# Kernel optimization log

Measured on AMD Instinct MI355X. Metric: run time of the kernel, lower is better.

The kernel has to match this reference:

```python
import jax, jax.numpy as jnp
import numpy as np

N, E = 50000, 800000
H, C = 4, 32          # heads, channels -> concat dim 128
ED = 8                # edge_dim
NREL = 16             # n_relations
LAYERS = 3
MLP_HID = 100
NEG_SLOPE = 0.2


def setup_inputs():
    key = jax.random.key(0)
    ks = jax.random.split(key, 16)
    s = 0.1
    return {
        "x": jax.random.normal(ks[0], (N, 1), jnp.float32),
        "edge_index": jax.random.randint(ks[1], (2, E), 0, N),
        "edge_type": jax.random.randint(ks[2], (E,), 0, NREL),
        "edge_emb": jax.random.normal(ks[3], (NREL, ED), jnp.float32) * s,
        "W_l0": jax.random.normal(ks[4], (C, H * C), jnp.float32) * s,
        "W_l1": jax.random.normal(ks[5], (H * C, H * C), jnp.float32) * s,
        "W_l2": jax.random.normal(ks[6], (H * C, H * C), jnp.float32) * s,
        "att_src": jax.random.normal(ks[7], (LAYERS, H, C), jnp.float32) * s,
        "att_dst": jax.random.normal(ks[8], (LAYERS, H, C), jnp.float32) * s,
        "att_edge": jax.random.normal(ks[9], (LAYERS, H, C), jnp.float32) * s,
        "W_edge": jax.random.normal(ks[10], (LAYERS, ED, H * C), jnp.float32) * s,
        "bias": jax.random.normal(ks[11], (LAYERS, H * C), jnp.float32) * s,
        "mlp_W1": jax.random.normal(ks[12], (H * C, MLP_HID), jnp.float32) * s,
        "mlp_b1": jnp.zeros((MLP_HID,), jnp.float32),
        "mlp_W2": jax.random.normal(ks[13], (MLP_HID, 1), jnp.float32) * s,
        "mlp_b2": jnp.zeros((1,), jnp.float32),
    }


def _gat_layer(x, src, dst, edge_attr, W, a_src, a_dst, a_edge, We, b):
    # PyG GATConv: shared lin for src/dst, additive attention + edge attr term
    n = x.shape[0]
    h = (x @ W).reshape(n, H, C)                      # [N,H,C]
    e = (edge_attr @ We).reshape(-1, H, C)            # [E',H,C]
    s_src = (h * a_src).sum(-1)                       # [N,H]
    s_dst = (h * a_dst).sum(-1)                       # [N,H]
    s_edge = (e * a_edge).sum(-1)                     # [E',H]
    alpha = jax.nn.leaky_relu(s_src[src] + s_dst[dst] + s_edge, NEG_SLOPE)
    # softmax over incoming edges of each destination node
    amax = jax.ops.segment_max(alpha, dst, num_segments=n)
    ealpha = jnp.exp(alpha - amax[dst])
    denom = jax.ops.segment_sum(ealpha, dst, num_segments=n)
    alpha = ealpha / (denom[dst] + 1e-16)             # [E',H]
    msg = h[src] * alpha[:, :, None]                  # [E',H,C]
    out = jax.ops.segment_sum(msg, dst, num_segments=n)
    return out.reshape(n, H * C) + b


def _forward(x, edge_index, edge_type, edge_emb, W_l0, W_l1, W_l2,
             att_src, att_dst, att_edge, W_edge, bias,
             mlp_W1, mlp_b1, mlp_W2, mlp_b2):
    n = x.shape[0]
    x = jnp.broadcast_to(x, (n, C))                   # x.expand(-1, channels)
    src, dst = edge_index[0], edge_index[1]
    loop = jnp.arange(n)
    src_f = jnp.concatenate([src, loop])              # add_self_loops
    dst_f = jnp.concatenate([dst, loop])
    Ws = [W_l0, W_l1, W_l2]
    for i in range(LAYERS):
        edge_attr = edge_emb[edge_type]               # [E,ED]
        fill = jnp.broadcast_to(edge_attr.mean(0), (n, ED))  # fill_value='mean'
        edge_attr_f = jnp.concatenate([edge_attr, fill], axis=0)
        xl = x
        x = _gat_layer(x, src_f, dst_f, edge_attr_f, Ws[i],
                       att_src[i], att_dst[i], att_edge[i], W_edge[i], bias[i])
        if i > 0:
            x = x + xl                                # residual (i>0 only)
        x = jax.nn.relu(x)                            # nonlin; norm='none'
    h = jax.nn.relu(x @ mlp_W1 + mlp_b1)
    return jax.nn.sigmoid(h @ mlp_W2 + mlp_b2)        # [N,1]


def reference(x, edge_index, edge_type, edge_emb, W_l0, W_l1, W_l2,
              att_src, att_dst, att_edge, W_edge, bias,
              mlp_W1, mlp_b1, mlp_W2, mlp_b2):
    return _forward(x, edge_index, edge_type, edge_emb, W_l0, W_l1, W_l2,
                    att_src, att_dst, att_edge, W_edge, bias,
                    mlp_W1, mlp_b1, mlp_W2, mlp_b2)
```

## Files before the change

kernel.cpp:

```cpp
#include <hip/hip_runtime.h>
#include <hip/hip_bf16.h>
#include <hip/hip_fp16.h>

#define HCONC 128
#define NHEAD 4
#define CCH   32
#define EDIM  8
#define NREL  16
#define BCAP  5120
#define TILE  2048

typedef float floatx2 __attribute__((ext_vector_type(2)));
typedef short bf16x8 __attribute__((ext_vector_type(8)));
typedef float f32x4 __attribute__((ext_vector_type(4)));

__device__ inline unsigned short pack_fp8x2(float a, float b) {
    return (unsigned short)(__builtin_amdgcn_cvt_pk_fp8_f32(a, b, 0, false) & 0xFFFF);
}
__device__ inline unsigned pack_bf2(float lo, float hi) {
    __hip_bfloat162 v;
    v.x = __float2bfloat16(lo);
    v.y = __float2bfloat16(hi);
    return *(unsigned*)&v;
}

__global__ __launch_bounds__(256) void binA_kernel(
    const int* __restrict__ ei, const int* __restrict__ etype, int E, int nbuk, int nA,
    int* __restrict__ gcursor, int* __restrict__ cnt, unsigned* __restrict__ ebuf,
    const float* __restrict__ W_l1, const float* __restrict__ W_l2,
    const float* __restrict__ mW1,
    unsigned* __restrict__ Wl1q, unsigned* __restrict__ Wl2q, unsigned* __restrict__ W1q,
    const float* __restrict__ W_l0, const float* __restrict__ emb,
    const float* __restrict__ att_src, const float* __restrict__ att_dst,
    const float* __restrict__ att_edge, const float* __restrict__ W_edge,
    float* __restrict__ W0s, float* __restrict__ SA0, float* __restrict__ SD0,
    float* __restrict__ stab) {
    __shared__ int hist[256], lbase[256], gbase[256], tmp[256];
    __shared__ int lcnt16[NREL];
    __shared__ unsigned srt[TILE];
    __shared__ unsigned char sbuk[TILE];
    __shared__ float W0s_s[HCONC];
    int t = threadIdx.x;

    if ((int)blockIdx.x >= nA) {
        int pb = (int)blockIdx.x - nA;
        if (pb == 92) {
            if (t < HCONC) {
                float s = 0.f;
                for (int k = 0; k < CCH; k++) s += W_l0[k * HCONC + t];
                W0s[t] = s; W0s_s[t] = s;
            }
            __syncthreads();
            if (t < NHEAD) {
                float sa = 0.f, sd = 0.f;
                for (int c = 0; c < CCH; c++) {
                    sa += W0s_s[t * CCH + c] * att_src[t * CCH + c];
                    sd += W0s_s[t * CCH + c] * att_dst[t * CCH + c];
                }
                SA0[t] = sa; SD0[t] = sd;
            }
            if (t < 192) {
                int l = t >> 6, rem = t & 63, typ = rem >> 2, hh = rem & 3;
                const float* attr = emb + typ * EDIM;
                const float* We = W_edge + l * EDIM * HCONC;
                const float* ae = att_edge + l * HCONC + hh * CCH;
                float s = 0.f;
                for (int c = 0; c < CCH; c++) {
                    float ev = 0.f;
                    for (int dd = 0; dd < EDIM; dd++)
                        ev += attr[dd] * We[dd * HCONC + hh * CCH + c];
                    s += ev * ae[c];
                }
                stab[l * 68 + typ * 4 + hh] = s;
            }
            return;
        }
        int i = pb * 256 + t;
        if (i < 16384) {
            const float* W = (i < 8192) ? W_l1 : W_l2;
            unsigned* dst = (i < 8192) ? Wl1q : Wl2q;
            int r = i & 8191;
            int j2 = r & 3, lane = (r >> 2) & 63, kb = (r >> 8) & 3, tt = r >> 10;
            int k0 = kb * 32 + ((lane >> 4) & 3) * 8 + 2 * j2;
            int c = 16 * tt + (lane & 15);
            dst[r] = pack_bf2(W[k0 * 128 + c], W[(k0 + 1) * 128 + c]);
        } else if (i < 16384 + 7168) {
            int r = i - 16384;
            int j2 = r & 3, lane = (r >> 2) & 63, kb = (r >> 8) & 3, tt = r >> 10;
            int k0 = kb * 32 + ((lane >> 4) & 3) * 8 + 2 * j2;
            int c = 16 * tt + (lane & 15);
            float lo = (c < 100) ? mW1[k0 * 100 + c] : 0.f;
            float hi = (c < 100) ? mW1[(k0 + 1) * 100 + c] : 0.f;
            W1q[r] = pack_bf2(lo, hi);
        }
        return;
    }

    hist[t] = 0;
    if (t < NREL) lcnt16[t] = 0;
    __syncthreads();

    int base = blockIdx.x * TILE;
    int count = min(TILE, E - base);

    unsigned rec[8]; int slot[8]; int buk[8];
#pragma unroll
    for (int i = 0; i < 8; i++) {
        int idx = t + i * 256;
        if (idx < count) {
            int g = base + idx;
            int s = ei[g], d = ei[E + g], ty = etype[g];
            rec[i] = (unsigned)s | ((unsigned)ty << 16) | ((unsigned)(d & 255) << 20);
            buk[i] = d >> 8;
            slot[i] = atomicAdd(&hist[buk[i]], 1);
            atomicAdd(&lcnt16[ty], 1);
        } else buk[i] = -1;
    }
    __syncthreads();

    int v = hist[t];
    tmp[t] = v; __syncthreads();
    for (int off = 1; off < 256; off <<= 1) {
        int add = (t >= off) ? tmp[t - off] : 0; __syncthreads();
        tmp[t] += add; __syncthreads();
    }
    lbase[t] = tmp[t] - v;
    if (t < nbuk && v > 0) gbase[t] = atomicAdd(&gcursor[t], v);
    __syncthreads();

#pragma unroll
    for (int i = 0; i < 8; i++)
        if (buk[i] >= 0) {
            int pos = lbase[buk[i]] + slot[i];
            srt[pos] = rec[i];
            sbuk[pos] = (unsigned char)buk[i];
        }
    if (t < NREL) atomicAdd(&cnt[t], lcnt16[t]);
    __syncthreads();

    for (int idx = t; idx < count; idx += 256) {
        unsigned r = srt[idx];
        int bk = sbuk[idx];
        int rel = gbase[bk] + idx - lbase[bk];
        if (rel < BCAP) ebuf[bk * BCAP + rel] = r;
    }
}

__global__ __launch_bounds__(256) void binB_kernel(
    const unsigned* __restrict__ ebuf, const int* __restrict__ gcursor,
    int n, int nbuk,
    int* __restrict__ row_ptr, unsigned* __restrict__ col,
    const int* __restrict__ cnt, float* __restrict__ stab, int E,
    const float* __restrict__ x,
    const float* __restrict__ SA0, const float* __restrict__ SD0,
    float* __restrict__ val0) {
    __shared__ int hist[256], lcur[256], tmp[256];
    __shared__ unsigned colsl[BCAP];
    __shared__ __align__(16) float stab0[68];
    int b = blockIdx.x, t = threadIdx.x;

    if (t < 64) stab0[t] = stab[t];
    float invE = 1.f / (float)E;
    if (t < 4) {
        float s = 0.f;
        for (int r = 0; r < NREL; r++) s += (float)cnt[r] * stab[r * 4 + t];
        stab0[64 + t] = s * invE;
    }

    int c = (t < nbuk) ? gcursor[t] : 0;
    tmp[t] = c; __syncthreads();
    for (int off = 1; off < 256; off <<= 1) {
        int add = (t >= off) ? tmp[t - off] : 0; __syncthreads();
        tmp[t] += add; __syncthreads();
    }
    int gstart = (b == 0) ? 0 : tmp[b - 1];
    if (b == 0 && t == nbuk - 1) row_ptr[n] = tmp[t];
    if (b == 0 && t < 12) {
        int l = t >> 2, hh = t & 3;
        float s = 0.f;
        for (int r = 0; r < NREL; r++) s += (float)cnt[r] * stab[l * 68 + r * 4 + hh];
        stab[l * 68 + 64 + hh] = s * invE;
    }
    __syncthreads();

    int bbase = b * BCAP;
    int cntb = min(gcursor[b], BCAP);
    hist[t] = 0;
    __syncthreads();
    for (int i = t; i < cntb; i += 256) {
        unsigned r = ebuf[bbase + i];
        atomicAdd(&hist[r >> 20], 1);
    }
    __syncthreads();
    int v = hist[t];
    tmp[t] = v; __syncthreads();
    for (int off = 1; off < 256; off <<= 1) {
        int add = (t >= off) ? tmp[t - off] : 0; __syncthreads();
        tmp[t] += add; __syncthreads();
    }
    lcur[t] = tmp[t] - v;
    int gdst = (b << 8) + t;
    if (gdst < n) row_ptr[gdst] = gstart + tmp[t] - v;
    __syncthreads();
    for (int i = t; i < cntb; i += 256) {
        unsigned r = ebuf[bbase + i];
        int pos = atomicAdd(&lcur[r >> 20], 1);
        colsl[pos] = r & 0xFFFFFu;
    }
    __syncthreads();
    for (int i = t; i < cntb; i += 256)
        col[gstart + i] = colsl[i];

    int lo = tmp[t] - v, hi = tmp[t];
    if (gdst < n) {
        float xd = x[gdst];
        float4 sa4 = *(const float4*)SA0;
        float4 sdc = *(const float4*)SD0;
        float sd0 = xd * sdc.x, sd1 = xd * sdc.y, sd2 = xd * sdc.z, sd3 = xd * sdc.w;
        float s0 = fmaf(xd, sa4.x, sd0) + stab0[64];
        float s1 = fmaf(xd, sa4.y, sd1) + stab0[65];
        float s2 = fmaf(xd, sa4.z, sd2) + stab0[66];
        float s3 = fmaf(xd, sa4.w, sd3) + stab0[67];
        s0 = s0 > 0.f ? s0 : 0.2f * s0;
        s1 = s1 > 0.f ? s1 : 0.2f * s1;
        s2 = s2 > 0.f ? s2 : 0.2f * s2;
        s3 = s3 > 0.f ? s3 : 0.2f * s3;
        float w0 = __expf(s0), w1 = __expf(s1), w2 = __expf(s2), w3 = __expf(s3);
        float den0 = w0, den1 = w1, den2 = w2, den3 = w3;
        float sx0 = w0 * xd, sx1 = w1 * xd, sx2 = w2 * xd, sx3 = w3 * xd;
        for (int j = lo; j < hi; j++) {
            unsigned p = colsl[j];
            float xv = x[p & 0xFFFFu];
            int typ = (int)(p >> 16);
            float4 st = *(const float4*)&stab0[typ * 4];
            float e0 = fmaf(xv, sa4.x, sd0) + st.x;
            float e1 = fmaf(xv, sa4.y, sd1) + st.y;
            float e2 = fmaf(xv, sa4.z, sd2) + st.z;
            float e3 = fmaf(xv, sa4.w, sd3) + st.w;
            e0 = e0 > 0.f ? e0 : 0.2f * e0;
            e1 = e1 > 0.f ? e1 : 0.2f * e1;
            e2 = e2 > 0.f ? e2 : 0.2f * e2;
            e3 = e3 > 0.f ? e3 : 0.2f * e3;
            float g0 = __expf(e0), g1 = __expf(e1), g2 = __expf(e2), g3 = __expf(e3);
            den0 += g0; den1 += g1; den2 += g2; den3 += g3;
            sx0 = fmaf(g0, xv, sx0); sx1 = fmaf(g1, xv, sx1);
            sx2 = fmaf(g2, xv, sx2); sx3 = fmaf(g3, xv, sx3);
        }
        float4 vo;
        vo.x = sx0 / (den0 + 1e-16f);
        vo.y = sx1 / (den1 + 1e-16f);
        vo.z = sx2 / (den2 + 1e-16f);
        vo.w = sx3 / (den3 + 1e-16f);
        ((float4*)val0)[gdst] = vo;
    }
}

__global__ __launch_bounds__(256, 2) void transform0_kernel(
    const float* __restrict__ val0, const float* __restrict__ W0s,
    const float* __restrict__ bias0, const unsigned* __restrict__ Wq,
    const float* __restrict__ a_src, const float* __restrict__ a_dst,
    unsigned short* __restrict__ h8, float* __restrict__ s_src,
    float* __restrict__ s_dst, int n) {
    __shared__ unsigned short hs[64 * 128];
    int tid = threadIdx.x;
    int lane = tid & 63;
    int wv = tid >> 6;
    int q = lane >> 4, nl = lane & 15;
    int row_blk = blockIdx.x * 64;
    int wrow = wv * 16;

    int arow = row_blk + wrow + nl;
    if (arow >= n) arow = n - 1;
    float4 v4 = ((const float4*)val0)[arow];

    f32x4 acc[8];
#pragma unroll
    for (int t = 0; t < 8; t++) acc[t] = (f32x4){0.f, 0.f, 0.f, 0.f};

    const uint4* Wp4 = (const uint4*)Wq;
#pragma unroll
    for (int kb = 0; kb < 4; kb++) {
        int c4 = 8 * kb + 2 * q;
        float4 wa = ((const float4*)W0s)[c4];
        float4 wb = ((const float4*)W0s)[c4 + 1];
        float4 ba = ((const float4*)bias0)[c4];
        float4 bb = ((const float4*)bias0)[c4 + 1];
        float vr = kb == 0 ? v4.x : kb == 1 ? v4.y : kb == 2 ? v4.z : v4.w;
        float x0 = fmaxf(fmaf(vr, wa.x, ba.x), 0.f);
        float x1 = fmaxf(fmaf(vr, wa.y, ba.y), 0.f);
        float x2 = fmaxf(fmaf(vr, wa.z, ba.z), 0.f);
        float x3 = fmaxf(fmaf(vr, wa.w, ba.w), 0.f);
        float x4 = fmaxf(fmaf(vr, wb.x, bb.x), 0.f);
        float x5 = fmaxf(fmaf(vr, wb.y, bb.y), 0.f);
        float x6 = fmaxf(fmaf(vr, wb.z, bb.z), 0.f);
        float x7 = fmaxf(fmaf(vr, wb.w, bb.w), 0.f);
        uint4 ua;
        ua.x = pack_bf2(x0, x1);
        ua.y = pack_bf2(x2, x3);
        ua.z = pack_bf2(x4, x5);
        ua.w = pack_bf2(x6, x7);
        bf16x8 af = __builtin_bit_cast(bf16x8, ua);
#pragma unroll
        for (int t = 0; t < 8; t++) {
            uint4 ub = Wp4[(t * 4 + kb) * 64 + lane];
            bf16x8 bf = __builtin_bit_cast(bf16x8, ub);
            acc[t] = __builtin_amdgcn_mfma_f32_16x16x32_bf16(af, bf, acc[t], 0, 0, 0);
        }
    }

    float av[8], dv[8];
#pragma unroll
    for (int t = 0; t < 8; t++) {
        av[t] = a_src[16 * t + nl];
        dv[t] = a_dst[16 * t + nl];
    }
#pragma unroll
    for (int reg = 0; reg < 4; reg++) {
        float t0 = acc[0][reg] * av[0] + acc[1][reg] * av[1];
        float t1 = acc[2][reg] * av[2] + acc[3][reg] * av[3];
        float t2 = acc[4][reg] * av[4] + acc[5][reg] * av[5];
        float t3 = acc[6][reg] * av[6] + acc[7][reg] * av[7];
        float d0 = acc[0][reg] * dv[0] + acc[1][reg] * dv[1];
        float d1 = acc[2][reg] * dv[2] + acc[3][reg] * dv[3];
        float d2 = acc[4][reg] * dv[4] + acc[5][reg] * dv[5];
        float d3 = acc[6][reg] * dv[6] + acc[7][reg] * dv[7];
#pragma unroll
        for (int off = 1; off <= 8; off <<= 1) {
            t0 += __shfl_xor(t0, off); t1 += __shfl_xor(t1, off);
            t2 += __shfl_xor(t2, off); t3 += __shfl_xor(t3, off);
            d0 += __shfl_xor(d0, off); d1 += __shfl_xor(d1, off);
            d2 += __shfl_xor(d2, off); d3 += __shfl_xor(d3, off);
        }
        int row = row_blk + wrow + q * 4 + reg;
        if (row < n && nl < 4) {
            float ts = nl == 0 ? t0 : nl == 1 ? t1 : nl == 2 ? t2 : t3;
            float td = nl == 0 ? d0 : nl == 1 ? d1 : nl == 2 ? d2 : d3;
            s_src[row * 4 + nl] = ts;
            s_dst[row * 4 + nl] = td;
        }
    }

#pragma unroll
    for (int t = 0; t < 8; t++) {
#pragma unroll
        for (int reg = 0; reg < 4; reg++) {
            __hip_bfloat16 b = __float2bfloat16(acc[t][reg]);
            hs[(wrow + q * 4 + reg) * 128 + 16 * t + nl] = *(unsigned short*)&b;
        }
    }
    __syncthreads();
    const unsigned* hsu = (const unsigned*)hs;
#pragma unroll
    for (int i = 0; i < 16; i++) {
        int pidx = tid + i * 256;
        int rl = pidx >> 6, cp = pidx & 63;
        int row = row_blk + rl;
        if (row < n) {
            unsigned u = hsu[rl * 64 + cp];
            float f0 = __uint_as_float(u << 16);
            float f1 = __uint_as_float(u & 0xFFFF0000u);
            h8[(size_t)row * 64 + cp] = pack_fp8x2(f0, f1);
        }
    }
}

__global__ __launch_bounds__(256) void agg_t_kernel(
    const unsigned char* __restrict__ h8, const float* __restrict__ s_src,
    const float* __restrict__ s_dst, const int* __restrict__ row_ptr,
    const unsigned* __restrict__ col, const float* __restrict__ tab,
    const float* __restrict__ bias, const float* __restrict__ val0,
    const float* __restrict__ W0s, const float* __restrict__ bias0,
    unsigned short* __restrict__ xb_out,
    const unsigned* __restrict__ Wq,
    const float* __restrict__ a_src2, const float* __restrict__ a_dst2,
    unsigned short* __restrict__ h8o, float* __restrict__ s_srco,
    float* __restrict__ s_dsto, int n) {
    __shared__ __align__(16) float stab_s[68];
    __shared__ __align__(16) unsigned short xrow[16 * 144];
    __shared__ __align__(4) unsigned short hs[16 * 130];
    if (threadIdx.x < 68) stab_s[threadIdx.x] = tab[threadIdx.x];
    __syncthreads();

    int tid = threadIdx.x;
    int lane = tid & 63;
    int wv = tid >> 6;
    int grp = lane >> 4;
    int l16 = lane & 15;
    int head = l16 >> 2;
    int dl = wv * 4 + grp;
    int d = blockIdx.x * 16 + dl;
    bool alive = d < n;
    int dc = alive ? d : n - 1;

    int start = row_ptr[dc];
    int end = alive ? row_ptr[dc + 1] : start;
    float sdh = s_dst[dc * 4 + head];

    float s = s_src[dc * 4 + head] + sdh + stab_s[64 + head];
    s = s > 0.f ? s : 0.2f * s;
    float w = __expf(s);
    uint2 u = ((const uint2*)(h8 + (size_t)dc * 128))[l16];
    floatx2 f01 = __builtin_amdgcn_cvt_pk_f32_fp8((int)u.x, false);
    floatx2 f23 = __builtin_amdgcn_cvt_pk_f32_fp8((int)u.x, true);
    floatx2 f45 = __builtin_amdgcn_cvt_pk_f32_fp8((int)u.y, false);
    floatx2 f67 = __builtin_amdgcn_cvt_pk_f32_fp8((int)u.y, true);
    float den = w;
    float a0 = w * f01.x, a1 = w * f01.y;
    float a2 = w * f23.x, a3 = w * f23.y;
    float a4 = w * f45.x, a5 = w * f45.y;
    float a6 = w * f67.x, a7 = w * f67.y;
#pragma unroll 4
    for (int e = start; e < end; e++) {
        unsigned pp = col[e];
        int esrc = (int)(pp & 0xFFFFu);
        int typ = (int)(pp >> 16);
        float sc = s_src[esrc * 4 + head] + sdh + stab_s[typ * 4 + head];
        sc = sc > 0.f ? sc : 0.2f * sc;
        float we = __expf(sc);
        uint2 ue = ((const uint2*)(h8 + (size_t)esrc * 128))[l16];
        floatx2 g01 = __builtin_amdgcn_cvt_pk_f32_fp8((int)ue.x, false);
        floatx2 g23 = __builtin_amdgcn_cvt_pk_f32_fp8((int)ue.x, true);
        floatx2 g45 = __builtin_amdgcn_cvt_pk_f32_fp8((int)ue.y, false);
        floatx2 g67 = __builtin_amdgcn_cvt_pk_f32_fp8((int)ue.y, true);
        den += we;
        a0 = fmaf(we, g01.x, a0);  a1 = fmaf(we, g01.y, a1);
        a2 = fmaf(we, g23.x, a2);  a3 = fmaf(we, g23.y, a3);
        a4 = fmaf(we, g45.x, a4);  a5 = fmaf(we, g45.y, a5);
        a6 = fmaf(we, g67.x, a6);  a7 = fmaf(we, g67.y, a7);
    }

    float inv = 1.f / (den + 1e-16f);
    float4 b0 = ((const float4*)bias)[2 * l16];
    float4 b1v = ((const float4*)bias)[2 * l16 + 1];
    float4 o0v, o1v;
    o0v.x = a0 * inv + b0.x;  o0v.y = a1 * inv + b0.y;
    o0v.z = a2 * inv + b0.z;  o0v.w = a3 * inv + b0.w;
    o1v.x = a4 * inv + b1v.x; o1v.y = a5 * inv + b1v.y;
    o1v.z = a6 * inv + b1v.z; o1v.w = a7 * inv + b1v.w;
    {
        float vv = val0[dc * 4 + head];
        float4 wa = ((const float4*)W0s)[2 * l16];
        float4 wb = ((const float4*)W0s)[2 * l16 + 1];
        float4 ba = ((const float4*)bias0)[2 * l16];
        float4 bb = ((const float4*)bias0)[2 * l16 + 1];
        o0v.x += fmaxf(fmaf(vv, wa.x, ba.x), 0.f);
        o0v.y += fmaxf(fmaf(vv, wa.y, ba.y), 0.f);
        o0v.z += fmaxf(fmaf(vv, wa.z, ba.z), 0.f);
        o0v.w += fmaxf(fmaf(vv, wa.w, ba.w), 0.f);
        o1v.x += fmaxf(fmaf(vv, wb.x, bb.x), 0.f);
        o1v.y += fmaxf(fmaf(vv, wb.y, bb.y), 0.f);
        o1v.z += fmaxf(fmaf(vv, wb.z, bb.z), 0.f);
        o1v.w += fmaxf(fmaf(vv, wb.w, bb.w), 0.f);
    }
    o0v.x = fmaxf(o0v.x, 0.f); o0v.y = fmaxf(o0v.y, 0.f);
    o0v.z = fmaxf(o0v.z, 0.f); o0v.w = fmaxf(o0v.w, 0.f);
    o1v.x = fmaxf(o1v.x, 0.f); o1v.y = fmaxf(o1v.y, 0.f);
    o1v.z = fmaxf(o1v.z, 0.f); o1v.w = fmaxf(o1v.w, 0.f);
    uint4 pk;
    pk.x = pack_bf2(o0v.x, o0v.y);
    pk.y = pack_bf2(o0v.z, o0v.w);
    pk.z = pack_bf2(o1v.x, o1v.y);
    pk.w = pack_bf2(o1v.z, o1v.w);
    if (alive) ((uint4*)xb_out)[(size_t)d * 16 + l16] = pk;
    *(uint4*)&xrow[dl * 144 + l16 * 8] = pk;
    __syncthreads();

    int lo = 2 * wv, hi = lo + 1;
    f32x4 aL = (f32x4){0.f, 0.f, 0.f, 0.f};
    f32x4 aH = (f32x4){0.f, 0.f, 0.f, 0.f};
    const uint4* Wp4 = (const uint4*)Wq;
#pragma unroll
    for (int kb = 0; kb < 4; kb++) {
        bf16x8 af = __builtin_bit_cast(bf16x8,
            *(const uint4*)&xrow[l16 * 144 + kb * 32 + grp * 8]);
        bf16x8 bL = __builtin_bit_cast(bf16x8, Wp4[(lo * 4 + kb) * 64 + lane]);
        bf16x8 bH = __builtin_bit_cast(bf16x8, Wp4[(hi * 4 + kb) * 64 + lane]);
        aL = __builtin_amdgcn_mfma_f32_16x16x32_bf16(af, bL, aL, 0, 0, 0);
        aH = __builtin_amdgcn_mfma_f32_16x16x32_bf16(af, bH, aH, 0, 0, 0);
    }
    float avl = a_src2[32 * wv + l16], avh = a_src2[32 * wv + 16 + l16];
    float dvl = a_dst2[32 * wv + l16], dvh = a_dst2[32 * wv + 16 + l16];
#pragma unroll
    for (int reg = 0; reg < 4; reg++) {
        float ps = aL[reg] * avl + aH[reg] * avh;
        float pd = aL[reg] * dvl + aH[reg] * dvh;
#pragma unroll
        for (int off = 1; off <= 8; off <<= 1) {
            ps += __shfl_xor(ps, off);
            pd += __shfl_xor(pd, off);
        }
        int rg = blockIdx.x * 16 + grp * 4 + reg;
        if (l16 == 0 && rg < n) {
            s_srco[rg * 4 + wv] = ps;
            s_dsto[rg * 4 + wv] = pd;
        }
        __hip_bfloat16 bLh = __float2bfloat16(aL[reg]);
        __hip_bfloat16 bHh = __float2bfloat16(aH[reg]);
        hs[(grp * 4 + reg) * 130 + 16 * lo + l16] = *(unsigned short*)&bLh;
        hs[(grp * 4 + reg) * 130 + 16 * hi + l16] = *(unsigned short*)&bHh;
    }
    __syncthreads();
#pragma unroll
    for (int i = 0; i < 4; i++) {
        int pidx = tid + i * 256;
        int rl = pidx >> 6, cp = pidx & 63;
        int rg = blockIdx.x * 16 + rl;
        if (rg < n) {
            unsigned uu = *(const unsigned*)&hs[rl * 130 + cp * 2];
            float f0 = __uint_as_float(uu << 16);
            float f1 = __uint_as_float(uu & 0xFFFF0000u);
            h8o[(size_t)rg * 64 + cp] = pack_fp8x2(f0, f1);
        }
    }
}

__global__ __launch_bounds__(256) void agg_m_kernel(
    const unsigned char* __restrict__ h8, const float* __restrict__ s_src,
    const float* __restrict__ s_dst, const int* __restrict__ row_ptr,
    const unsigned* __restrict__ col, const float* __restrict__ tab,
    const float* __restrict__ bias, const unsigned short* __restrict__ x_prev,
    const unsigned* __restrict__ W1q, const float* __restrict__ b1,
    const float* __restrict__ W2, const float* __restrict__ b2,
    float* __restrict__ out, int n) {
    __shared__ __align__(16) float stab_s[68];
    __shared__ __align__(16) unsigned short xrow[16 * 144];
    __shared__ float partial[16][4];
    if (threadIdx.x < 68) stab_s[threadIdx.x] = tab[threadIdx.x];
    __syncthreads();

    int tid = threadIdx.x;
    int lane = tid & 63;
    int wv = tid >> 6;
    int grp = lane >> 4;
    int l16 = lane & 15;
    int head = l16 >> 2;
    int dl = wv * 4 + grp;
    int d = blockIdx.x * 16 + dl;
    bool alive = d < n;
    int dc = alive ? d : n - 1;

    int start = row_ptr[dc];
    int end = alive ? row_ptr[dc + 1] : start;
    float sdh = s_dst[dc * 4 + head];

    float s = s_src[dc * 4 + head] + sdh + stab_s[64 + head];
    s = s > 0.f ? s : 0.2f * s;
    float w = __expf(s);
    uint2 u = ((const uint2*)(h8 + (size_t)dc * 128))[l16];
    floatx2 f01 = __builtin_amdgcn_cvt_pk_f32_fp8((int)u.x, false);
    floatx2 f23 = __builtin_amdgcn_cvt_pk_f32_fp8((int)u.x, true);
    floatx2 f45 = __builtin_amdgcn_cvt_pk_f32_fp8((int)u.y, false);
    floatx2 f67 = __builtin_amdgcn_cvt_pk_f32_fp8((int)u.y, true);
    float den = w;
    float a0 = w * f01.x, a1 = w * f01.y;
    float a2 = w * f23.x, a3 = w * f23.y;
    float a4 = w * f45.x, a5 = w * f45.y;
    float a6 = w * f67.x, a7 = w * f67.y;
#pragma unroll 4
    for (int e = start; e < end; e++) {
        unsigned pp = col[e];
        int esrc = (int)(pp & 0xFFFFu);
        int typ = (int)(pp >> 16);
        float sc = s_src[esrc * 4 + head] + sdh + stab_s[typ * 4 + head];
        sc = sc > 0.f ? sc : 0.2f * sc;
        float we = __expf(sc);
        uint2 ue = ((const uint2*)(h8 + (size_t)esrc * 128))[l16];
        floatx2 g01 = __builtin_amdgcn_cvt_pk_f32_fp8((int)ue.x, false);
        floatx2 g23 = __builtin_amdgcn_cvt_pk_f32_fp8((int)ue.x, true);
        floatx2 g45 = __builtin_amdgcn_cvt_pk_f32_fp8((int)ue.y, false);
        floatx2 g67 = __builtin_amdgcn_cvt_pk_f32_fp8((int)ue.y, true);
        den += we;
        a0 = fmaf(we, g01.x, a0);  a1 = fmaf(we, g01.y, a1);
        a2 = fmaf(we, g23.x, a2);  a3 = fmaf(we, g23.y, a3);
        a4 = fmaf(we, g45.x, a4);  a5 = fmaf(we, g45.y, a5);
        a6 = fmaf(we, g67.x, a6);  a7 = fmaf(we, g67.y, a7);
    }

    float inv = 1.f / (den + 1e-16f);
    float4 b0 = ((const float4*)bias)[2 * l16];
    float4 b1v = ((const float4*)bias)[2 * l16 + 1];
    float4 o0v, o1v;
    o0v.x = a0 * inv + b0.x;  o0v.y = a1 * inv + b0.y;
    o0v.z = a2 * inv + b0.z;  o0v.w = a3 * inv + b0.w;
    o1v.x = a4 * inv + b1v.x; o1v.y = a5 * inv + b1v.y;
    o1v.z = a6 * inv + b1v.z; o1v.w = a7 * inv + b1v.w;
    {
        uint4 pr = ((const uint4*)x_prev)[(size_t)dc * 16 + l16];
        o0v.x += __uint_as_float(pr.x << 16);
        o0v.y += __uint_as_float(pr.x & 0xFFFF0000u);
        o0v.z += __uint_as_float(pr.y << 16);
        o0v.w += __uint_as_float(pr.y & 0xFFFF0000u);
        o1v.x += __uint_as_float(pr.z << 16);
        o1v.y += __uint_as_float(pr.z & 0xFFFF0000u);
        o1v.z += __uint_as_float(pr.w << 16);
        o1v.w += __uint_as_float(pr.w & 0xFFFF0000u);
    }
    o0v.x = fmaxf(o0v.x, 0.f); o0v.y = fmaxf(o0v.y, 0.f);
    o0v.z = fmaxf(o0v.z, 0.f); o0v.w = fmaxf(o0v.w, 0.f);
    o1v.x = fmaxf(o1v.x, 0.f); o1v.y = fmaxf(o1v.y, 0.f);
    o1v.z = fmaxf(o1v.z, 0.f); o1v.w = fmaxf(o1v.w, 0.f);
    uint4 pk;
    pk.x = pack_bf2(o0v.x, o0v.y);
    pk.y = pack_bf2(o0v.z, o0v.w);
    pk.z = pack_bf2(o1v.x, o1v.y);
    pk.w = pack_bf2(o1v.z, o1v.w);
    *(uint4*)&xrow[dl * 144 + l16 * 8] = pk;
    __syncthreads();

    int lo = 2 * wv;
    bool two = wv < 3;
    f32x4 aL = (f32x4){0.f, 0.f, 0.f, 0.f};
    f32x4 aH = (f32x4){0.f, 0.f, 0.f, 0.f};
    const uint4* Wp4 = (const uint4*)W1q;
#pragma unroll
    for (int kb = 0; kb < 4; kb++) {
        bf16x8 af = __builtin_bit_cast(bf16x8,
            *(const uint4*)&xrow[l16 * 144 + kb * 32 + grp * 8]);
        bf16x8 bL = __builtin_bit_cast(bf16x8, Wp4[(lo * 4 + kb) * 64 + lane]);
        aL = __builtin_amdgcn_mfma_f32_16x16x32_bf16(af, bL, aL, 0, 0, 0);
        if (two) {
            bf16x8 bH = __builtin_bit_cast(bf16x8, Wp4[((lo + 1) * 4 + kb) * 64 + lane]);
            aH = __builtin_amdgcn_mfma_f32_16x16x32_bf16(af, bH, aH, 0, 0, 0);
        }
    }
    int cL = 16 * lo + l16;
    float b1L = (cL < 100) ? b1[cL] : 0.f;
    float w2L = (cL < 100) ? W2[cL] : 0.f;
    float b1H = 0.f, w2H = 0.f;
    if (two) {
        int cH = cL + 16;
        b1H = (cH < 100) ? b1[cH] : 0.f;
        w2H = (cH < 100) ? W2[cH] : 0.f;
    }
#pragma unroll
    for (int reg = 0; reg < 4; reg++) {
        float psum = fmaxf(aL[reg] + b1L, 0.f) * w2L;
        if (two) psum = fmaf(fmaxf(aH[reg] + b1H, 0.f), w2H, psum);
#pragma unroll
        for (int off = 1; off <= 8; off <<= 1)
            psum += __shfl_xor(psum, off);
        if (l16 == 0) partial[grp * 4 + reg][wv] = psum;
    }
    __syncthreads();
    if (tid < 16) {
        int rg = blockIdx.x * 16 + tid;
        if (rg < n) {
            float sum = partial[tid][0] + partial[tid][1] +
                        partial[tid][2] + partial[tid][3] + b2[0];
            out[rg] = 1.f / (1.f + __expf(-sum));
        }
    }
}

extern "C" void kernel_launch(void* const* d_in, const int* in_sizes, int n_in,
                              void* d_out, int out_size, void* d_ws, size_t ws_size,
                              hipStream_t stream) {
    const float* x       = (const float*)d_in[0];
    const int*   ei      = (const int*)d_in[1];
    const int*   etype   = (const int*)d_in[2];
    const float* emb     = (const float*)d_in[3];
    const float* W_l0    = (const float*)d_in[4];
    const float* W_l1    = (const float*)d_in[5];
    const float* W_l2    = (const float*)d_in[6];
    const float* att_src = (const float*)d_in[7];
    const float* att_dst = (const float*)d_in[8];
    const float* att_edge= (const float*)d_in[9];
    const float* W_edge  = (const float*)d_in[10];
    const float* bias    = (const float*)d_in[11];
    const float* mW1     = (const float*)d_in[12];
    const float* mb1     = (const float*)d_in[13];
    const float* mW2     = (const float*)d_in[14];
    const float* mb2     = (const float*)d_in[15];

    int n = in_sizes[0];
    int E = in_sizes[2];
    int nbuk = (n + 255) >> 8;
    int nA = (E + TILE - 1) / TILE;

    float* p   = (float*)d_ws;
    float* xb  = p; p += (size_t)n * 64;
    float* ssrc = p; p += (size_t)n * NHEAD;
    float* sdst = p; p += (size_t)n * NHEAD;
    float* ssrc2 = p; p += (size_t)n * NHEAD;
    float* sdst2 = p; p += (size_t)n * NHEAD;
    float* val0 = p; p += (size_t)n * NHEAD;
    float* hbf  = p; p += (size_t)n * 32;
    float* hbf2 = p; p += (size_t)n * 32;
    unsigned* Wl1q = (unsigned*)p; p += 8192;
    unsigned* Wl2q = (unsigned*)p; p += 8192;
    unsigned* W1q  = (unsigned*)p; p += 7168;
    int* row_ptr     = (int*)p;
    int* gcursor     = row_ptr + n + 1;
    int* cnt         = gcursor + 256;
    float* W0s    = (float*)(cnt + 16);
    float* SA0    = W0s + HCONC;
    float* SD0    = SA0 + NHEAD;
    float* meanat = SD0 + NHEAD;
    float* stab   = meanat + EDIM;
    char* raw = (char*)(stab + 256);
    unsigned* ebuf = (unsigned*)(((uintptr_t)raw + 15) & ~(uintptr_t)15);
    unsigned* col = ebuf + (size_t)nbuk * BCAP;

    (void)hipMemsetAsync(gcursor, 0, (256 + 16) * sizeof(int), stream);
    binA_kernel<<<nA + 93, 256, 0, stream>>>(ei, etype, E, nbuk, nA, gcursor, cnt,
                                             ebuf, W_l1, W_l2, mW1, Wl1q, Wl2q, W1q,
                                             W_l0, emb, att_src, att_dst, att_edge,
                                             W_edge, W0s, SA0, SD0, stab);
    binB_kernel<<<nbuk, 256, 0, stream>>>(ebuf, gcursor, n, nbuk, row_ptr, col,
                                          cnt, stab, E, x, SA0, SD0, val0);

    transform0_kernel<<<(n + 63) / 64, 256, 0, stream>>>(val0, W0s, bias + 0, Wl1q,
                                                         att_src + 128, att_dst + 128,
                                                         (unsigned short*)hbf, ssrc, sdst, n);
    agg_t_kernel<<<(n + 15) / 16, 256, 0, stream>>>(
        (const unsigned char*)hbf, ssrc, sdst, row_ptr, col,
        stab + 68, bias + 128, val0, W0s, bias + 0,
        (unsigned short*)xb, Wl2q, att_src + 256, att_dst + 256,
        (unsigned short*)hbf2, ssrc2, sdst2, n);
    agg_m_kernel<<<(n + 15) / 16, 256, 0, stream>>>(
        (const unsigned char*)hbf2, ssrc2, sdst2, row_ptr, col,
        stab + 136, bias + 256, (const unsigned short*)xb,
        W1q, mb1, mW2, mb2, (float*)d_out, n);
}
```

Before: 202.7 us.

## Fuse layer-0 transform into binning kernel and stage edge columns in LDS

The separate transform0 kernel is merged into binB. Each binB block keeps its 256 layer-0 aggregated values in shared memory and runs the MFMA transform over four 64-row phases, which removes one launch and the val0 reload. The agg_t and agg_m kernels also preload their block's contiguous column-index range into shared memory (up to 1024 entries) before the edge loop. In exchange, binB uses more LDS and runs with only 196 blocks, which limits parallelism for the transform work. The aggregation kernels also gain an extra barrier and a per-edge branch.

```diff
diff --git a/kernel.cpp b/kernel.cpp
--- a/kernel.cpp
+++ b/kernel.cpp
@@ -9,6 +9,7 @@
 #define NREL  16
 #define BCAP  5120
 #define TILE  2048
+#define CCAP  1024
 
 typedef float floatx2 __attribute__((ext_vector_type(2)));
 typedef short bf16x8 __attribute__((ext_vector_type(8)));
@@ -153,10 +154,18 @@
     const int* __restrict__ cnt, float* __restrict__ stab, int E,
     const float* __restrict__ x,
     const float* __restrict__ SA0, const float* __restrict__ SD0,
-    float* __restrict__ val0) {
+    float* __restrict__ val0,
+    const float* __restrict__ W0s, const float* __restrict__ bias0,
+    const unsigned* __restrict__ Wq,
+    const float* __restrict__ a_src, const float* __restrict__ a_dst,
+    unsigned short* __restrict__ h8, float* __restrict__ s_src,
+    float* __restrict__ s_dst) {
     __shared__ int hist[256], lcur[256], tmp[256];
     __shared__ unsigned colsl[BCAP];
     __shared__ __align__(16) float stab0[68];
+    __shared__ __align__(16) float vls[256][4];
+    __shared__ __align__(16) float W0s_s[HCONC], b0_s[HCONC];
+    __shared__ unsigned short hs[64 * 128];
     int b = blockIdx.x, t = threadIdx.x;
 
     if (t < 64) stab0[t] = stab[t];
@@ -166,6 +175,7 @@
         for (int r = 0; r < NREL; r++) s += (float)cnt[r] * stab[r * 4 + t];
         stab0[64 + t] = s * invE;
     }
+    if (t < HCONC) { W0s_s[t] = W0s[t]; b0_s[t] = bias0[t]; }
 
     int c = (t < nbuk) ? gcursor[t] : 0;
     tmp[t] = c; __syncthreads();
@@ -211,7 +221,8 @@
     for (int i = t; i < cntb; i += 256)
         col[gstart + i] = colsl[i];
 
-    int lo = tmp[t] - v, hi = tmp[t];
+    int lo0 = tmp[t] - v, hi0 = tmp[t];
+    float4 vo = make_float4(0.f, 0.f, 0.f, 0.f);
     if (gdst < n) {
         float xd = x[gdst];
         float4 sa4 = *(const float4*)SA0;
@@ -228,7 +239,7 @@
         float w0 = __expf(s0), w1 = __expf(s1), w2 = __expf(s2), w3 = __expf(s3);
         float den0 = w0, den1 = w1, den2 = w2, den3 = w3;
         float sx0 = w0 * xd, sx1 = w1 * xd, sx2 = w2 * xd, sx3 = w3 * xd;
-        for (int j = lo; j < hi; j++) {
+        for (int j = lo0; j < hi0; j++) {
             unsigned p = colsl[j];
             float xv = x[p & 0xFFFFu];
             int typ = (int)(p >> 16);
@@ -246,121 +257,111 @@
             sx0 = fmaf(g0, xv, sx0); sx1 = fmaf(g1, xv, sx1);
             sx2 = fmaf(g2, xv, sx2); sx3 = fmaf(g3, xv, sx3);
         }
-        float4 vo;
         vo.x = sx0 / (den0 + 1e-16f);
         vo.y = sx1 / (den1 + 1e-16f);
         vo.z = sx2 / (den2 + 1e-16f);
         vo.w = sx3 / (den3 + 1e-16f);
         ((float4*)val0)[gdst] = vo;
     }
-}
-
-__global__ __launch_bounds__(256, 2) void transform0_kernel(
-    const float* __restrict__ val0, const float* __restrict__ W0s,
-    const float* __restrict__ bias0, const unsigned* __restrict__ Wq,
-    const float* __restrict__ a_src, const float* __restrict__ a_dst,
-    unsigned short* __restrict__ h8, float* __restrict__ s_src,
-    float* __restrict__ s_dst, int n) {
-    __shared__ unsigned short hs[64 * 128];
-    int tid = threadIdx.x;
-    int lane = tid & 63;
-    int wv = tid >> 6;
+    *(float4*)vls[t] = vo;
+    __syncthreads();
+
+    int lane = t & 63, wvv = t >> 6;
     int q = lane >> 4, nl = lane & 15;
-    int row_blk = blockIdx.x * 64;
-    int wrow = wv * 16;
-
-    int arow = row_blk + wrow + nl;
-    if (arow >= n) arow = n - 1;
-    float4 v4 = ((const float4*)val0)[arow];
-
-    f32x4 acc[8];
-#pragma unroll
-    for (int t = 0; t < 8; t++) acc[t] = (f32x4){0.f, 0.f, 0.f, 0.f};
-
     const uint4* Wp4 = (const uint4*)Wq;
-#pragma unroll
-    for (int kb = 0; kb < 4; kb++) {
-        int c4 = 8 * kb + 2 * q;
-        float4 wa = ((const float4*)W0s)[c4];
-        float4 wb = ((const float4*)W0s)[c4 + 1];
-        float4 ba = ((const float4*)bias0)[c4];
-        float4 bb = ((const float4*)bias0)[c4 + 1];
-        float vr = kb == 0 ? v4.x : kb == 1 ? v4.y : kb == 2 ? v4.z : v4.w;
-        float x0 = fmaxf(fmaf(vr, wa.x, ba.x), 0.f);
-        float x1 = fmaxf(fmaf(vr, wa.y, ba.y), 0.f);
-        float x2 = fmaxf(fmaf(vr, wa.z, ba.z), 0.f);
-        float x3 = fmaxf(fmaf(vr, wa.w, ba.w), 0.f);
-        float x4 = fmaxf(fmaf(vr, wb.x, bb.x), 0.f);
-        float x5 = fmaxf(fmaf(vr, wb.y, bb.y), 0.f);
-        float x6 = fmaxf(fmaf(vr, wb.z, bb.z), 0.f);
-        float x7 = fmaxf(fmaf(vr, wb.w, bb.w), 0.f);
-        uint4 ua;
-        ua.x = pack_bf2(x0, x1);
-        ua.y = pack_bf2(x2, x3);
-        ua.z = pack_bf2(x4, x5);
-        ua.w = pack_bf2(x6, x7);
-        bf16x8 af = __builtin_bit_cast(bf16x8, ua);
-#pragma unroll
-        for (int t = 0; t < 8; t++) {
-            uint4 ub = Wp4[(t * 4 + kb) * 64 + lane];
-            bf16x8 bf = __builtin_bit_cast(bf16x8, ub);
-            acc[t] = __builtin_amdgcn_mfma_f32_16x16x32_bf16(af, bf, acc[t], 0, 0, 0);
-        }
-    }
-
     float av[8], dv[8];
 #pragma unroll
-    for (int t = 0; t < 8; t++) {
-        av[t] = a_src[16 * t + nl];
-        dv[t] = a_dst[16 * t + nl];
-    }
-#pragma unroll
-    for (int reg = 0; reg < 4; reg++) {
-        float t0 = acc[0][reg] * av[0] + acc[1][reg] * av[1];
-        float t1 = acc[2][reg] * av[2] + acc[3][reg] * av[3];
-        float t2 = acc[4][reg] * av[4] + acc[5][reg] * av[5];
-        float t3 = acc[6][reg] * av[6] + acc[7][reg] * av[7];
-        float d0 = acc[0][reg] * dv[0] + acc[1][reg] * dv[1];
-        float d1 = acc[2][reg] * dv[2] + acc[3][reg] * dv[3];
-        float d2 = acc[4][reg] * dv[4] + acc[5][reg] * dv[5];
-        float d3 = acc[6][reg] * dv[6] + acc[7][reg] * dv[7];
-#pragma unroll
-        for (int off = 1; off <= 8; off <<= 1) {
-            t0 += __shfl_xor(t0, off); t1 += __shfl_xor(t1, off);
-            t2 += __shfl_xor(t2, off); t3 += __shfl_xor(t3, off);
-            d0 += __shfl_xor(d0, off); d1 += __shfl_xor(d1, off);
-            d2 += __shfl_xor(d2, off); d3 += __shfl_xor(d3, off);
-        }
-        int row = row_blk + wrow + q * 4 + reg;
-        if (row < n && nl < 4) {
-            float ts = nl == 0 ? t0 : nl == 1 ? t1 : nl == 2 ? t2 : t3;
-            float td = nl == 0 ? d0 : nl == 1 ? d1 : nl == 2 ? d2 : d3;
-            s_src[row * 4 + nl] = ts;
-            s_dst[row * 4 + nl] = td;
-        }
-    }
-
-#pragma unroll
-    for (int t = 0; t < 8; t++) {
+    for (int tt = 0; tt < 8; tt++) {
+        av[tt] = a_src[16 * tt + nl];
+        dv[tt] = a_dst[16 * tt + nl];
+    }
+    for (int ph = 0; ph < 4; ph++) {
+        int wrow = wvv * 16;
+        int lrow = ph * 64 + wrow + nl;
+        float4 v4 = *(const float4*)vls[lrow];
+
+        f32x4 acc[8];
+#pragma unroll
+        for (int tt = 0; tt < 8; tt++) acc[tt] = (f32x4){0.f, 0.f, 0.f, 0.f};
+#pragma unroll
+        for (int kb = 0; kb < 4; kb++) {
+            int c4 = 8 * kb + 2 * q;
+            float4 wa = ((const float4*)W0s_s)[c4];
+            float4 wb = ((const float4*)W0s_s)[c4 + 1];
+            float4 ba = ((const float4*)b0_s)[c4];
+            float4 bb = ((const float4*)b0_s)[c4 + 1];
+            float vr = kb == 0 ? v4.x : kb == 1 ? v4.y : kb == 2 ? v4.z : v4.w;
+            float x0 = fmaxf(fmaf(vr, wa.x, ba.x), 0.f);
+            float x1 = fmaxf(fmaf(vr, wa.y, ba.y), 0.f);
+            float x2 = fmaxf(fmaf(vr, wa.z, ba.z), 0.f);
+            float x3 = fmaxf(fmaf(vr, wa.w, ba.w), 0.f);
+            float x4 = fmaxf(fmaf(vr, wb.x, bb.x), 0.f);
+            float x5 = fmaxf(fmaf(vr, wb.y, bb.y), 0.f);
+            float x6 = fmaxf(fmaf(vr, wb.z, bb.z), 0.f);
+            float x7 = fmaxf(fmaf(vr, wb.w, bb.w), 0.f);
+            uint4 ua;
+            ua.x = pack_bf2(x0, x1);
+            ua.y = pack_bf2(x2, x3);
+            ua.z = pack_bf2(x4, x5);
+            ua.w = pack_bf2(x6, x7);
+            bf16x8 af = __builtin_bit_cast(bf16x8, ua);
+#pragma unroll
+            for (int tt = 0; tt < 8; tt++) {
+                uint4 ub = Wp4[(tt * 4 + kb) * 64 + lane];
+                bf16x8 bf = __builtin_bit_cast(bf16x8, ub);
+                acc[tt] = __builtin_amdgcn_mfma_f32_16x16x32_bf16(af, bf, acc[tt], 0, 0, 0);
+            }
+        }
+
 #pragma unroll
         for (int reg = 0; reg < 4; reg++) {
-            __hip_bfloat16 b = __float2bfloat16(acc[t][reg]);
-            hs[(wrow + q * 4 + reg) * 128 + 16 * t + nl] = *(unsigned short*)&b;
-        }
-    }
-    __syncthreads();
-    const unsigned* hsu = (const unsigned*)hs;
-#pragma unroll
-    for (int i = 0; i < 16; i++) {
-        int pidx = tid + i * 256;
-        int rl = pidx >> 6, cp = pidx & 63;
-        int row = row_blk + rl;
-        if (row < n) {
-            unsigned u = hsu[rl * 64 + cp];
-            float f0 = __uint_as_float(u << 16);
-            float f1 = __uint_as_float(u & 0xFFFF0000u);
-            h8[(size_t)row * 64 + cp] = pack_fp8x2(f0, f1);
-        }
+            float t0 = acc[0][reg] * av[0] + acc[1][reg] * av[1];
+            float t1 = acc[2][reg] * av[2] + acc[3][reg] * av[3];
+            float t2 = acc[4][reg] * av[4] + acc[5][reg] * av[5];
+            float t3 = acc[6][reg] * av[6] + acc[7][reg] * av[7];
+            float d0 = acc[0][reg] * dv[0] + acc[1][reg] * dv[1];
+            float d1 = acc[2][reg] * dv[2] + acc[3][reg] * dv[3];
+            float d2 = acc[4][reg] * dv[4] + acc[5][reg] * dv[5];
+            float d3 = acc[6][reg] * dv[6] + acc[7][reg] * dv[7];
+#pragma unroll
+            for (int off = 1; off <= 8; off <<= 1) {
+                t0 += __shfl_xor(t0, off); t1 += __shfl_xor(t1, off);
+                t2 += __shfl_xor(t2, off); t3 += __shfl_xor(t3, off);
+                d0 += __shfl_xor(d0, off); d1 += __shfl_xor(d1, off);
+                d2 += __shfl_xor(d2, off); d3 += __shfl_xor(d3, off);
+            }
+            int grow = (b << 8) + ph * 64 + wrow + q * 4 + reg;
+            if (grow < n && nl < 4) {
+                float ts = nl == 0 ? t0 : nl == 1 ? t1 : nl == 2 ? t2 : t3;
+                float td = nl == 0 ? d0 : nl == 1 ? d1 : nl == 2 ? d2 : d3;
+                s_src[grow * 4 + nl] = ts;
+                s_dst[grow * 4 + nl] = td;
+            }
+        }
+
+#pragma unroll
+        for (int tt = 0; tt < 8; tt++) {
+#pragma unroll
+            for (int reg = 0; reg < 4; reg++) {
+                __hip_bfloat16 bh = __float2bfloat16(acc[tt][reg]);
+                hs[(wrow + q * 4 + reg) * 128 + 16 * tt + nl] = *(unsigned short*)&bh;
+            }
+        }
+        __syncthreads();
+        const unsigned* hsu = (const unsigned*)hs;
+#pragma unroll
+        for (int i = 0; i < 16; i++) {
+            int pidx = t + i * 256;
+            int rl = pidx >> 6, cp = pidx & 63;
+            int grow = (b << 8) + ph * 64 + rl;
+            if (grow < n) {
+                unsigned u = hsu[rl * 64 + cp];
+                float f0 = __uint_as_float(u << 16);
+                float f1 = __uint_as_float(u & 0xFFFF0000u);
+                h8[(size_t)grow * 64 + cp] = pack_fp8x2(f0, f1);
+            }
+        }
+        __syncthreads();
     }
 }
 
@@ -378,10 +379,21 @@
     __shared__ __align__(16) float stab_s[68];
     __shared__ __align__(16) unsigned short xrow[16 * 144];
     __shared__ __align__(4) unsigned short hs[16 * 130];
-    if (threadIdx.x < 68) stab_s[threadIdx.x] = tab[threadIdx.x];
-    __syncthreads();
-
+    __shared__ unsigned cols_s[CCAP];
+    __shared__ int ebb[2];
     int tid = threadIdx.x;
+    if (tid < 68) stab_s[tid] = tab[tid];
+    if (tid < 2) {
+        int ridx = (int)blockIdx.x * 16 + tid * 16;
+        if (ridx > n) ridx = n;
+        ebb[tid] = row_ptr[ridx];
+    }
+    __syncthreads();
+    int ebase = ebb[0];
+    int etot = ebb[1] - ebase;
+    for (int i = tid; i < etot && i < CCAP; i += 256) cols_s[i] = col[ebase + i];
+    __syncthreads();
+
     int lane = tid & 63;
     int wv = tid >> 6;
     int grp = lane >> 4;
@@ -411,7 +423,8 @@
     float a6 = w * f67.x, a7 = w * f67.y;
 #pragma unroll 4
     for (int e = start; e < end; e++) {
-        unsigned pp = col[e];
+        int ei_ = e - ebase;
+        unsigned pp = (ei_ < CCAP) ? cols_s[ei_] : col[e];
         int esrc = (int)(pp & 0xFFFFu);
         int typ = (int)(pp >> 16);
         float sc = s_src[esrc * 4 + head] + sdh + stab_s[typ * 4 + head];
@@ -525,10 +538,21 @@
     __shared__ __align__(16) float stab_s[68];
     __shared__ __align__(16) unsigned short xrow[16 * 144];
     __shared__ float partial[16][4];
-    if (threadIdx.x < 68) stab_s[threadIdx.x] = tab[threadIdx.x];
-    __syncthreads();
-
+    __shared__ unsigned cols_s[CCAP];
+    __shared__ int ebb[2];
     int tid = threadIdx.x;
+    if (tid < 68) stab_s[tid] = tab[tid];
+    if (tid < 2) {
+        int ridx = (int)blockIdx.x * 16 + tid * 16;
+        if (ridx > n) ridx = n;
+        ebb[tid] = row_ptr[ridx];
+    }
+    __syncthreads();
+    int ebase = ebb[0];
+    int etot = ebb[1] - ebase;
+    for (int i = tid; i < etot && i < CCAP; i += 256) cols_s[i] = col[ebase + i];
+    __syncthreads();
+
     int lane = tid & 63;
     int wv = tid >> 6;
     int grp = lane >> 4;
@@ -558,7 +582,8 @@
     float a6 = w * f67.x, a7 = w * f67.y;
 #pragma unroll 4
     for (int e = start; e < end; e++) {
-        unsigned pp = col[e];
+        int ei_ = e - ebase;
+        unsigned pp = (ei_ < CCAP) ? cols_s[ei_] : col[e];
         int esrc = (int)(pp & 0xFFFFu);
         int typ = (int)(pp >> 16);
         float sc = s_src[esrc * 4 + head] + sdh + stab_s[typ * 4 + head];
@@ -707,11 +732,11 @@
                                              W_l0, emb, att_src, att_dst, att_edge,
                                              W_edge, W0s, SA0, SD0, stab);
     binB_kernel<<<nbuk, 256, 0, stream>>>(ebuf, gcursor, n, nbuk, row_ptr, col,
-                                          cnt, stab, E, x, SA0, SD0, val0);
-
-    transform0_kernel<<<(n + 63) / 64, 256, 0, stream>>>(val0, W0s, bias + 0, Wl1q,
-                                                         att_src + 128, att_dst + 128,
-                                                         (unsigned short*)hbf, ssrc, sdst, n);
+                                          cnt, stab, E, x, SA0, SD0, val0,
+                                          W0s, bias + 0, Wl1q,
+                                          att_src + 128, att_dst + 128,
+                                          (unsigned short*)hbf, ssrc, sdst);
+
     agg_t_kernel<<<(n + 15) / 16, 256, 0, stream>>>(
         (const unsigned char*)hbf, ssrc, sdst, row_ptr, col,
         stab + 68, bias + 128, val0, W0s, bias + 0,
```

New measurement: 203.8 us, median of 2. Within noise of the previous version (+0.5%).
